# Kernel tuning notes

Hardware: AMD Instinct MI355X
Metric: run time of the kernel (lower is better)

The kernel has to match this reference:

```python
import jax, jax.numpy as jnp
import numpy as np

B, S = 2, 2048
IN, CD = 512, 128
HID, HEADS, DH = 1024, 8, 128
FFN, LAT, L = 4096, 256, 2


def _ln(x, s, b, eps=1e-5):
    m = x.mean(-1, keepdims=True)
    v = x.var(-1, keepdims=True)
    return (x - m) / jnp.sqrt(v + eps) * s + b


def _decay_mask():
    # D[h, n, m] = gamma_h^(n-m) for n >= m else 0; gamma_h = 1 - 2^(-5-h)
    n = jnp.arange(S)
    d = (n[:, None] - n[None, :]).astype(jnp.float32)
    mask = d >= 0
    expo = jnp.where(mask, d, 0.0)
    gammas = 1.0 - 2.0 ** (-5.0 - jnp.arange(HEADS, dtype=jnp.float32))
    return (gammas[:, None, None] ** expo[None]) * mask[None]


def setup_inputs() -> dict:
    key = jax.random.key(0)
    ks = jax.random.split(key, 20)
    f32 = jnp.float32
    def nrm(k, shape, s=0.02):
        return jax.random.normal(k, shape, f32) * s
    return {
        "x": jax.random.normal(ks[0], (B, S, IN), f32),
        "c": jax.random.normal(ks[1], (B, S, CD), f32),
        "W_in": nrm(ks[2], (IN + CD, HID)), "b_in": jnp.zeros((HID,), f32),
        "ln1_s": jnp.ones((L, HID), f32), "ln1_b": jnp.zeros((L, HID), f32),
        "Wq": nrm(ks[3], (L, HID, HID)), "Wk": nrm(ks[4], (L, HID, HID)),
        "Wv": nrm(ks[5], (L, HID, HID)), "Wg": nrm(ks[6], (L, HID, HID)),
        "Wo": nrm(ks[7], (L, HID, HID)),
        "gn_s": jnp.ones((L, HID), f32), "gn_b": jnp.zeros((L, HID), f32),
        "ln2_s": jnp.ones((L, HID), f32), "ln2_b": jnp.zeros((L, HID), f32),
        "W1": nrm(ks[8], (L, HID, FFN)), "b1": jnp.zeros((L, FFN), f32),
        "W2": nrm(ks[9], (L, FFN, HID)), "b2": jnp.zeros((L, HID), f32),
        "lnf_s": jnp.ones((HID,), f32), "lnf_b": jnp.zeros((HID,), f32),
        "W_mu": nrm(ks[10], (HID, LAT)), "b_mu": jnp.zeros((LAT,), f32),
        "W_lv": nrm(ks[11], (HID, LAT)), "b_lv": jnp.zeros((LAT,), f32),
    }


def reference(x, c, W_in, b_in, ln1_s, ln1_b, Wq, Wk, Wv, Wg, Wo, gn_s, gn_b,
              ln2_s, ln2_b, W1, b1, W2, b2, lnf_s, lnf_b, W_mu, b_mu, W_lv, b_lv):
    D = _decay_mask()                        # [H, S, S]
    h = jnp.concatenate([x, c], -1) @ W_in + b_in  # [B, S, HID]
    scale = 1.0 / np.sqrt(DH).astype(np.float32)
    for l in range(L):
        # --- multi-scale retention (parallel form) ---
        xn = _ln(h, ln1_s[l], ln1_b[l])
        q = (xn @ Wq[l]).reshape(B, S, HEADS, DH)
        k = (xn @ Wk[l]).reshape(B, S, HEADS, DH)
        v = (xn @ Wv[l]).reshape(B, S, HEADS, DH)
        scores = jnp.einsum('bnhd,bmhd->bhnm', q, k) * scale
        scores = scores * D[None]            # causal decay weighting
        o = jnp.einsum('bhnm,bmhd->bnhd', scores, v)
        # per-head group norm
        mu_ = o.mean(-1, keepdims=True)
        var_ = o.var(-1, keepdims=True)
        o = (o - mu_) / jnp.sqrt(var_ + 1e-5)
        o = o * gn_s[l].reshape(HEADS, DH) + gn_b[l].reshape(HEADS, DH)
        o = o.reshape(B, S, HID)
        g = jax.nn.silu(xn @ Wg[l])
        h = h + (g * o) @ Wo[l]
        # --- FFN ---
        xn2 = _ln(h, ln2_s[l], ln2_b[l])
        h = h + jax.nn.gelu(xn2 @ W1[l] + b1[l]) @ W2[l] + b2[l]
    h = _ln(h, lnf_s, lnf_b)
    mu = h @ W_mu + b_mu
    raw_logvar = h @ W_lv + b_lv
    std = jax.nn.softplus(0.5 * raw_logvar) + 0.001
    return mu, std
```

## Files before the change

kernel.cpp:

```cpp
#include <hip/hip_runtime.h>
#include <cmath>

typedef __bf16 bf16_t;
typedef __bf16 bf16x8 __attribute__((ext_vector_type(8)));
typedef float f32x4 __attribute__((ext_vector_type(4)));
typedef unsigned int u32x4 __attribute__((ext_vector_type(4)));

namespace {

constexpr int kS = 2048;
constexpr int kTok = 4096;
constexpr int kHid = 1024;
constexpr int kDh = 128;
constexpr float kScale = 0.08838834764831843f;

enum {
  EPI_BF16 = 0,
  EPI_BIAS_F32 = 2,
  EPI_RESID_F32 = 3,
  EPI_BIAS_GELU_BF16 = 4,
  EPI_MULV = 7,
  EPI_PART = 8,
};

__device__ __forceinline__ void gload16(const void* g, void* l) {
  __builtin_amdgcn_global_load_lds(
      (const __attribute__((address_space(1))) void*)g,
      (__attribute__((address_space(3))) void*)l, 16, 0, 0);
}

__global__ __launch_bounds__(256) void build_a0_kernel(
    const float* __restrict__ x, const float* __restrict__ c,
    bf16_t* __restrict__ a0)
{
  int i = blockIdx.x * 256 + threadIdx.x;
  if (i >= kTok * 640) return;
  int t = i / 640;
  int col = i - t * 640;
  float v = (col < 512) ? x[(size_t)t * 512 + col]
                        : c[(size_t)t * 128 + (col - 512)];
  a0[i] = (bf16_t)v;
}

__global__ __launch_bounds__(256) void transpose_cast_kernel(
    const float* __restrict__ src, bf16_t* __restrict__ dst, int K, int N)
{
  __shared__ float tile[32][33];
  int n0 = blockIdx.x * 32, k0 = blockIdx.y * 32;
  int tx = threadIdx.x, ty = threadIdx.y;
#pragma unroll
  for (int ii = 0; ii < 4; ++ii) {
    int r = ty + ii * 8;
    tile[r][tx] = src[(size_t)(k0 + r) * N + (n0 + tx)];
  }
  __syncthreads();
#pragma unroll
  for (int ii = 0; ii < 4; ++ii) {
    int r = ty + ii * 8;
    dst[(size_t)(n0 + r) * K + (k0 + tx)] = (bf16_t)tile[tx][r];
  }
}

__global__ __launch_bounds__(256) void head_transpose_kernel(
    const bf16_t* __restrict__ in, int ld, bf16_t* __restrict__ out)
{
  __shared__ bf16_t tile[32][33];
  int s0 = blockIdx.x * 32;
  int d0 = blockIdx.y * 32;
  int bh = blockIdx.z;
  int b = bh >> 3, h = bh & 7;
  int tx = threadIdx.x & 31, ty = threadIdx.x >> 5;
#pragma unroll
  for (int ii = 0; ii < 4; ++ii) {
    int r = ty + ii * 8;
    tile[r][tx] = in[(size_t)(b * kS + s0 + r) * ld + h * kDh + d0 + tx];
  }
  __syncthreads();
#pragma unroll
  for (int ii = 0; ii < 4; ++ii) {
    int r = ty + ii * 8;
    out[((size_t)bh * kDh + d0 + r) * kS + s0 + tx] = tile[tx][r];
  }
}

__global__ __launch_bounds__(256) void ln_kernel(
    const float* __restrict__ H, const float* __restrict__ s,
    const float* __restrict__ b, bf16_t* __restrict__ out)
{
  const int t = blockIdx.x;
  const int tid = threadIdx.x;
  const float* row = H + (size_t)t * kHid;
  f32x4 x = *(const f32x4*)(row + tid * 4);
  float sum = x[0] + x[1] + x[2] + x[3];
  float ssq = x[0]*x[0] + x[1]*x[1] + x[2]*x[2] + x[3]*x[3];
#pragma unroll
  for (int m = 32; m >= 1; m >>= 1) {
    sum += __shfl_xor(sum, m, 64);
    ssq += __shfl_xor(ssq, m, 64);
  }
  __shared__ float red[8];
  int wave = tid >> 6;
  if ((tid & 63) == 0) { red[wave] = sum; red[4 + wave] = ssq; }
  __syncthreads();
  sum = red[0] + red[1] + red[2] + red[3];
  ssq = red[4] + red[5] + red[6] + red[7];
  float mean = sum * (1.0f / kHid);
  float var = ssq * (1.0f / kHid) - mean * mean;
  float rstd = rsqrtf(var + 1e-5f);
  bf16_t* orow = out + (size_t)t * kHid;
#pragma unroll
  for (int j = 0; j < 4; ++j) {
    int col = tid * 4 + j;
    orow[col] = (bf16_t)((x[j] - mean) * rstd * s[col] + b[col]);
  }
}

__global__ __launch_bounds__(256) void gn_gate_kernel(
    const float* __restrict__ o, const float* __restrict__ gns,
    const float* __restrict__ gnb, bf16_t* __restrict__ g, int ldg)
{
  int idx = blockIdx.x * 4 + (threadIdx.x >> 6);
  int lane = threadIdx.x & 63;
  size_t off = (size_t)idx * kDh;
  float v0 = o[off + lane * 2];
  float v1 = o[off + lane * 2 + 1];
  float sum = v0 + v1, ssq = v0 * v0 + v1 * v1;
#pragma unroll
  for (int m = 32; m >= 1; m >>= 1) {
    sum += __shfl_xor(sum, m, 64);
    ssq += __shfl_xor(ssq, m, 64);
  }
  float mean = sum * (1.0f / kDh);
  float var = ssq * (1.0f / kDh) - mean * mean;
  float rstd = rsqrtf(var + 1e-5f);
  int t = idx >> 3, h = idx & 7;
  int c0 = h * kDh + lane * 2;
  float s0 = gns[c0], s1 = gns[c0 + 1], b0 = gnb[c0], b1 = gnb[c0 + 1];
  size_t goff = (size_t)t * ldg + h * kDh + lane * 2;
  float g0 = (float)g[goff], g1 = (float)g[goff + 1];
  g0 = g0 / (1.0f + __expf(-g0));
  g1 = g1 / (1.0f + __expf(-g1));
  g[goff]     = (bf16_t)(((v0 - mean) * rstd * s0 + b0) * g0);
  g[goff + 1] = (bf16_t)(((v1 - mean) * rstd * s1 + b1) * g1);
}

template <int TM, int EPI>
__global__ __launch_bounds__(256) void gemm_kernel(
    const bf16_t* __restrict__ A, int lda, const bf16_t* __restrict__ Bt, int ldb,
    void* __restrict__ Cv, int ldc, const float* __restrict__ bias,
    const float* __restrict__ bias2, const float* __restrict__ resid,
    int M, int N, int kSpan)
{
  constexpr int MR = TM / 32;
  constexpr int ASEG = TM / 8;
  constexpr int TOT = ASEG + 16;
  constexpr int PER_WAVE = TOT / 4;
  __shared__ bf16_t As[2][TM * 64];
  __shared__ bf16_t Bs[2][128 * 64];
  const int tid = threadIdx.x;
  const int lane = tid & 63;
  const int wave = tid >> 6;
  const int wr = (wave >> 1) * (MR * 16);
  const int wc = (wave & 1) * 64;
  const int bm = blockIdx.x * TM;
  const int bn = blockIdx.y * 128;
  const int kb = blockIdx.z * kSpan;
  const int r_ld = lane >> 3;
  const int cg = ((lane & 7) ^ r_ld) * 8;

  f32x4 acc[MR][4] = {};

  auto stage = [&](int bufi, int t) {
    int k0 = kb + t * 64;
#pragma unroll
    for (int i = 0; i < PER_WAVE; ++i) {
      int seg = wave * PER_WAVE + i;
      if (seg < ASEG) {
        int r = seg * 8 + r_ld;
        gload16(&A[(size_t)(bm + r) * lda + k0 + cg], &As[bufi][seg * 512]);
      } else {
        int s2 = seg - ASEG;
        int r = s2 * 8 + r_ld;
        gload16(&Bt[(size_t)(bn + r) * ldb + k0 + cg], &Bs[bufi][s2 * 512]);
      }
    }
  };
  auto compute = [&](int bufi) {
#pragma unroll
    for (int kk = 0; kk < 64; kk += 32) {
      const int cg0 = (kk >> 3) + (lane >> 4);
      bf16x8 af[MR], bfr[4];
#pragma unroll
      for (int m = 0; m < MR; ++m) {
        int row = wr + m * 16 + (lane & 15);
        af[m] = *(const bf16x8*)&As[bufi][row * 64 + ((cg0 ^ (row & 7)) << 3)];
      }
#pragma unroll
      for (int n = 0; n < 4; ++n) {
        int row = wc + n * 16 + (lane & 15);
        bfr[n] = *(const bf16x8*)&Bs[bufi][row * 64 + ((cg0 ^ (row & 7)) << 3)];
      }
#pragma unroll
      for (int m = 0; m < MR; ++m)
#pragma unroll
        for (int n = 0; n < 4; ++n)
          acc[m][n] = __builtin_amdgcn_mfma_f32_16x16x32_bf16(af[m], bfr[n], acc[m][n], 0, 0, 0);
    }
  };

  const int nt = kSpan >> 6;
  stage(0, 0);
  stage(1, 1);
  for (int t = 0; t < nt; ++t) {
    if (t + 1 < nt) {
      if constexpr (PER_WAVE == 8) asm volatile("s_waitcnt vmcnt(8)" ::: "memory");
      else                         asm volatile("s_waitcnt vmcnt(6)" ::: "memory");
    } else {
      asm volatile("s_waitcnt vmcnt(0)" ::: "memory");
    }
    __builtin_amdgcn_s_barrier();
    compute(t & 1);
    __builtin_amdgcn_s_barrier();
    if (t + 2 < nt) stage(t & 1, t + 2);
  }

  const int cr = (lane >> 4) * 4;
  const int cc = lane & 15;
#pragma unroll
  for (int m = 0; m < MR; ++m) {
#pragma unroll
    for (int n = 0; n < 4; ++n) {
#pragma unroll
      for (int j = 0; j < 4; ++j) {
        int gr = bm + wr + m * 16 + cr + j;
        int gc = bn + wc + n * 16 + cc;
        size_t off = (size_t)gr * ldc + gc;
        float v = acc[m][n][j];
        if constexpr (EPI == EPI_BF16) {
          ((bf16_t*)Cv)[off] = (bf16_t)v;
        } else if constexpr (EPI == EPI_BIAS_F32) {
          ((float*)Cv)[off] = v + bias[gc];
        } else if constexpr (EPI == EPI_RESID_F32) {
          ((float*)Cv)[off] = v + resid[off];
        } else if constexpr (EPI == EPI_BIAS_GELU_BF16) {
          v += bias[gc];
          float u3 = v + 0.044715f * v * v * v;
          float th = tanhf(0.7978845608028654f * u3);
          ((bf16_t*)Cv)[off] = (bf16_t)(0.5f * v * (1.0f + th));
        } else if constexpr (EPI == EPI_PART) {
          ((float*)Cv)[(size_t)blockIdx.z * M * N + off] = v;
        } else if constexpr (EPI == EPI_MULV) {
          if (gc < 256) {
            ((float*)Cv)[(size_t)gr * 256 + gc] = v + bias[gc];
          } else {
            float r2 = 0.5f * (v + bias2[gc - 256]);
            float sp = (r2 > 20.0f) ? r2 : log1pf(__expf(r2));
            ((float*)Cv)[(size_t)4096 * 256 + (size_t)gr * 256 + (gc - 256)] = sp + 0.001f;
          }
        }
      }
    }
  }
}

__global__ __launch_bounds__(256) void ffn2_reduce_kernel(
    const float* __restrict__ P, const float* __restrict__ b2,
    float* __restrict__ H)
{
  int i = blockIdx.x * 256 + threadIdx.x;
  size_t e = (size_t)i * 4;
  int col = (int)(e & 1023);
  f32x4 a = *(const f32x4*)&P[e];
  f32x4 b = *(const f32x4*)&P[(size_t)4096 * 1024 + e];
  f32x4 h = *(const f32x4*)&H[e];
  f32x4 bb = *(const f32x4*)&b2[col];
  f32x4 r = { h[0] + a[0] + b[0] + bb[0], h[1] + a[1] + b[1] + bb[1],
              h[2] + a[2] + b[2] + bb[2], h[3] + a[3] + b[3] + bb[3] };
  *(f32x4*)&H[e] = r;
}

__global__ __launch_bounds__(256) void chunk_state_kernel(
    const bf16_t* __restrict__ KT, const bf16_t* __restrict__ VT,
    bf16_t* __restrict__ U)
{
  __shared__ bf16_t Ka[128][72];
  __shared__ bf16_t Va[128][72];
  const int tid = threadIdx.x, lane = tid & 63, wave = tid >> 6;
  const int t = blockIdx.x, bh = blockIdx.y, h = bh & 7;
  const float lg2g = log2f(1.0f - exp2f(-5.0f - (float)h));
#pragma unroll
  for (int it = 0; it < 4; ++it) {
    int u = tid + it * 256;
    int r = u >> 3, cg = (u & 7) * 8;
    size_t g = ((size_t)bh * kDh + r) * kS + t * 64 + cg;
    *(u32x4*)&Va[r][cg] = *(const u32x4*)&VT[g];
    bf16x8 kv = *(const bf16x8*)&KT[g];
    bf16x8 ks;
#pragma unroll
    for (int j = 0; j < 8; ++j)
      ks[j] = (bf16_t)((float)kv[j] * exp2f((float)(63 - (cg + j)) * lg2g));
    *(bf16x8*)&Ka[r][cg] = ks;
  }
  __syncthreads();
  f32x4 acc[2][8] = {};
#pragma unroll
  for (int kk = 0; kk < 64; kk += 32) {
    bf16x8 af[2], bfr[8];
#pragma unroll
    for (int m = 0; m < 2; ++m)
      af[m] = *(const bf16x8*)&Va[wave * 32 + m * 16 + (lane & 15)][kk + (lane >> 4) * 8];
#pragma unroll
    for (int n = 0; n < 8; ++n)
      bfr[n] = *(const bf16x8*)&Ka[n * 16 + (lane & 15)][kk + (lane >> 4) * 8];
#pragma unroll
    for (int m = 0; m < 2; ++m)
#pragma unroll
      for (int n = 0; n < 8; ++n)
        acc[m][n] = __builtin_amdgcn_mfma_f32_16x16x32_bf16(af[m], bfr[n], acc[m][n], 0, 0, 0);
  }
  size_t base = ((size_t)bh * 32 + t) * 16384;
#pragma unroll
  for (int m = 0; m < 2; ++m)
#pragma unroll
    for (int n = 0; n < 8; ++n)
#pragma unroll
      for (int j = 0; j < 4; ++j) {
        int dv = wave * 32 + m * 16 + (lane >> 4) * 4 + j;
        int dk = n * 16 + (lane & 15);
        U[base + dv * 128 + dk] = (bf16_t)acc[m][n][j];
      }
}

__global__ __launch_bounds__(256) void chunk_scan_kernel(
    const bf16_t* __restrict__ U, bf16_t* __restrict__ S)
{
  int e = blockIdx.x * 256 + threadIdx.x;
  int bh = blockIdx.y, h = bh & 7;
  float d64 = exp2f(64.0f * log2f(1.0f - exp2f(-5.0f - (float)h)));
  float s = 0.0f;
  size_t base = (size_t)bh * 32 * 16384 + e;
  for (int t = 0; t < 32; ++t) {
    size_t idx = base + (size_t)t * 16384;
    float u = (float)U[idx];
    S[idx] = (bf16_t)s;
    s = d64 * s + u;
  }
}

__global__ __launch_bounds__(256) void chunk_out_kernel(
    const bf16_t* __restrict__ QB, const bf16_t* __restrict__ KB, int ldq,
    const bf16_t* __restrict__ VT, const bf16_t* __restrict__ S,
    float* __restrict__ OF)
{
  __shared__ bf16_t Qs[64][136];
  __shared__ bf16_t Ks[64][136];
  __shared__ bf16_t Vs[128][72];
  __shared__ bf16_t Ps[64][72];
  const int tid = threadIdx.x, lane = tid & 63, wave = tid >> 6;
  const int t = blockIdx.x, bh = blockIdx.y;
  const int b = bh >> 3, h = bh & 7;
  const float lg2g = log2f(1.0f - exp2f(-5.0f - (float)h));

#pragma unroll
  for (int it = 0; it < 4; ++it) {
    int u = tid + it * 256;
    int r = u >> 4, cg = (u & 15) * 8;
    size_t g = ((size_t)b * kS + t * 64 + r) * ldq + h * kDh + cg;
    *(u32x4*)&Qs[r][cg] = *(const u32x4*)&QB[g];
    *(u32x4*)&Ks[r][cg] = *(const u32x4*)&KB[g];
    int rv = u >> 3, cv = (u & 7) * 8;
    *(u32x4*)&Vs[rv][cv] = *(const u32x4*)&VT[((size_t)bh * kDh + rv) * kS + t * 64 + cv];
  }
  __syncthreads();

  f32x4 sf[4] = {};
#pragma unroll
  for (int kk = 0; kk < 128; kk += 32) {
    bf16x8 aq = *(const bf16x8*)&Qs[wave * 16 + (lane & 15)][kk + (lane >> 4) * 8];
#pragma unroll
    for (int c2 = 0; c2 < 4; ++c2) {
      bf16x8 bk = *(const bf16x8*)&Ks[c2 * 16 + (lane & 15)][kk + (lane >> 4) * 8];
      sf[c2] = __builtin_amdgcn_mfma_f32_16x16x32_bf16(aq, bk, sf[c2], 0, 0, 0);
    }
  }
#pragma unroll
  for (int c2 = 0; c2 < 4; ++c2)
#pragma unroll
    for (int j = 0; j < 4; ++j) {
      int nl = wave * 16 + (lane >> 4) * 4 + j;
      int ml = c2 * 16 + (lane & 15);
      int d = nl - ml;
      float w = (d >= 0) ? kScale * exp2f((float)d * lg2g) : 0.0f;
      Ps[nl][ml] = (bf16_t)(sf[c2][j] * w);
    }
  __syncthreads();

  f32x4 oa[8] = {}, oi[8] = {};
#pragma unroll
  for (int ks = 0; ks < 64; ks += 32) {
    bf16x8 ap = *(const bf16x8*)&Ps[wave * 16 + (lane & 15)][ks + (lane >> 4) * 8];
#pragma unroll
    for (int dt = 0; dt < 8; ++dt) {
      bf16x8 bv = *(const bf16x8*)&Vs[dt * 16 + (lane & 15)][ks + (lane >> 4) * 8];
      oa[dt] = __builtin_amdgcn_mfma_f32_16x16x32_bf16(ap, bv, oa[dt], 0, 0, 0);
    }
  }
  size_t sbase = ((size_t)bh * 32 + t) * 16384;
#pragma unroll
  for (int kk = 0; kk < 128; kk += 32) {
    bf16x8 aq = *(const bf16x8*)&Qs[wave * 16 + (lane & 15)][kk + (lane >> 4) * 8];
#pragma unroll
    for (int dt = 0; dt < 8; ++dt) {
      bf16x8 bs = *(const bf16x8*)&S[sbase + (size_t)(dt * 16 + (lane & 15)) * 128 + kk + (lane >> 4) * 8];
      oi[dt] = __builtin_amdgcn_mfma_f32_16x16x32_bf16(aq, bs, oi[dt], 0, 0, 0);
    }
  }
#pragma unroll
  for (int dt = 0; dt < 8; ++dt)
#pragma unroll
    for (int j = 0; j < 4; ++j) {
      int nl = wave * 16 + (lane >> 4) * 4 + j;
      float gf = kScale * exp2f((float)(nl + 1) * lg2g);
      OF[((size_t)b * kS + t * 64 + nl) * kHid + h * kDh + dt * 16 + (lane & 15)] =
          oa[dt][j] + gf * oi[dt][j];
    }
}

template <int TM>
void launch_gemm(int epi, const bf16_t* A, int lda, const bf16_t* Bt, int ldb,
                 void* C, int ldc, const float* bias, const float* bias2,
                 const float* resid, int M, int N, int K, int ksplit, hipStream_t st)
{
  dim3 g(M / TM, N / 128, ksplit), b(256);
  int kSpan = K / ksplit;
  switch (epi) {
    case EPI_BF16:           gemm_kernel<TM, EPI_BF16><<<g, b, 0, st>>>(A, lda, Bt, ldb, C, ldc, bias, bias2, resid, M, N, kSpan); break;
    case EPI_BIAS_F32:       gemm_kernel<TM, EPI_BIAS_F32><<<g, b, 0, st>>>(A, lda, Bt, ldb, C, ldc, bias, bias2, resid, M, N, kSpan); break;
    case EPI_RESID_F32:      gemm_kernel<TM, EPI_RESID_F32><<<g, b, 0, st>>>(A, lda, Bt, ldb, C, ldc, bias, bias2, resid, M, N, kSpan); break;
    case EPI_BIAS_GELU_BF16: gemm_kernel<TM, EPI_BIAS_GELU_BF16><<<g, b, 0, st>>>(A, lda, Bt, ldb, C, ldc, bias, bias2, resid, M, N, kSpan); break;
    case EPI_PART:           gemm_kernel<TM, EPI_PART><<<g, b, 0, st>>>(A, lda, Bt, ldb, C, ldc, bias, bias2, resid, M, N, kSpan); break;
    case EPI_MULV:           gemm_kernel<TM, EPI_MULV><<<g, b, 0, st>>>(A, lda, Bt, ldb, C, ldc, bias, bias2, resid, M, N, kSpan); break;
  }
}

void launch_transpose(const float* src, bf16_t* dst, int K, int N, hipStream_t st) {
  transpose_cast_kernel<<<dim3(N / 32, K / 32), dim3(32, 8), 0, st>>>(src, dst, K, N);
}

}

extern "C" void kernel_launch(void* const* d_in, const int* in_sizes, int n_in,
                              void* d_out, int out_size, void* d_ws, size_t ws_size,
                              hipStream_t stream) {
  const float* x     = (const float*)d_in[0];
  const float* c     = (const float*)d_in[1];
  const float* W_in  = (const float*)d_in[2];
  const float* b_in  = (const float*)d_in[3];
  const float* ln1_s = (const float*)d_in[4];
  const float* ln1_b = (const float*)d_in[5];
  const float* Wq    = (const float*)d_in[6];
  const float* Wk    = (const float*)d_in[7];
  const float* Wv    = (const float*)d_in[8];
  const float* Wg    = (const float*)d_in[9];
  const float* Wo    = (const float*)d_in[10];
  const float* gn_s  = (const float*)d_in[11];
  const float* gn_b  = (const float*)d_in[12];
  const float* ln2_s = (const float*)d_in[13];
  const float* ln2_b = (const float*)d_in[14];
  const float* W1    = (const float*)d_in[15];
  const float* b1    = (const float*)d_in[16];
  const float* W2    = (const float*)d_in[17];
  const float* b2    = (const float*)d_in[18];
  const float* lnf_s = (const float*)d_in[19];
  const float* lnf_b = (const float*)d_in[20];
  const float* W_mu  = (const float*)d_in[21];
  const float* b_mu  = (const float*)d_in[22];
  const float* W_lv  = (const float*)d_in[23];
  const float* b_lv  = (const float*)d_in[24];

  char* p = (char*)d_ws;
  bf16_t* WT   = (bf16_t*)p; p += (size_t)4096 * 1024 * 2;
  bf16_t* A0   = (bf16_t*)p; p += (size_t)4096 * 640 * 2;
  float*  H    = (float*) p; p += (size_t)4096 * 1024 * 4;
  bf16_t* XN   = (bf16_t*)p; p += (size_t)4096 * 1024 * 2;
  bf16_t* QKVG = (bf16_t*)p; p += (size_t)4096 * 4096 * 2;
  bf16_t* Sb   = (bf16_t*)p; p += (size_t)16 * 32 * 16384 * 2;
  float*  OF   = (float*) p; p += (size_t)4096 * 1024 * 4;
  bf16_t* F1 = QKVG;
  bf16_t* KT = WT;
  bf16_t* VT = XN;
  bf16_t* Ub = (bf16_t*)OF;
  float*  PART = (float*)Sb;

  build_a0_kernel<<<dim3((kTok * 640 + 255) / 256), dim3(256), 0, stream>>>(x, c, A0);
  launch_transpose(W_in, WT, 640, 1024, stream);
  launch_gemm<64>(EPI_BIAS_F32, A0, 640, WT, 640, H, 1024, b_in, nullptr, nullptr,
                  4096, 1024, 640, 1, stream);

  for (int l = 0; l < 2; ++l) {
    const size_t wsq = (size_t)l * 1024 * 1024;
    ln_kernel<<<dim3(4096), dim3(256), 0, stream>>>(H, ln1_s + l * 1024, ln1_b + l * 1024, XN);

    launch_transpose(Wq + wsq, WT,                      1024, 1024, stream);
    launch_transpose(Wk + wsq, WT + ((size_t)1 << 20),  1024, 1024, stream);
    launch_transpose(Wv + wsq, WT + ((size_t)2 << 20),  1024, 1024, stream);
    launch_transpose(Wg + wsq, WT + ((size_t)3 << 20),  1024, 1024, stream);
    launch_gemm<128>(EPI_BF16, XN, 1024, WT, 1024, QKVG, 4096, nullptr, nullptr, nullptr,
                     4096, 4096, 1024, 1, stream);

    head_transpose_kernel<<<dim3(64, 4, 16), dim3(256), 0, stream>>>(QKVG + 1024, 4096, KT);
    head_transpose_kernel<<<dim3(64, 4, 16), dim3(256), 0, stream>>>(QKVG + 2048, 4096, VT);
    chunk_state_kernel<<<dim3(32, 16), dim3(256), 0, stream>>>(KT, VT, Ub);
    chunk_scan_kernel<<<dim3(64, 16), dim3(256), 0, stream>>>(Ub, (bf16_t*)Sb);
    chunk_out_kernel<<<dim3(32, 16), dim3(256), 0, stream>>>(QKVG, QKVG + 1024, 4096, VT, (bf16_t*)Sb, OF);

    gn_gate_kernel<<<dim3(8192), dim3(256), 0, stream>>>(OF, gn_s + l * 1024, gn_b + l * 1024,
                                                         QKVG + 3072, 4096);

    launch_transpose(Wo + wsq, WT, 1024, 1024, stream);
    launch_gemm<64>(EPI_RESID_F32, QKVG + 3072, 4096, WT, 1024, H, 1024, nullptr, nullptr, H,
                    4096, 1024, 1024, 1, stream);

    ln_kernel<<<dim3(4096), dim3(256), 0, stream>>>(H, ln2_s + l * 1024, ln2_b + l * 1024, XN);
    launch_transpose(W1 + (size_t)l * 1024 * 4096, WT, 1024, 4096, stream);
    launch_gemm<128>(EPI_BIAS_GELU_BF16, XN, 1024, WT, 1024, F1, 4096, b1 + l * 4096, nullptr, nullptr,
                     4096, 4096, 1024, 1, stream);
    launch_transpose(W2 + (size_t)l * 4096 * 1024, WT, 4096, 1024, stream);
    launch_gemm<128>(EPI_PART, F1, 4096, WT, 4096, PART, 1024, nullptr, nullptr, nullptr,
                     4096, 1024, 4096, 2, stream);
    ffn2_reduce_kernel<<<dim3(4096), dim3(256), 0, stream>>>(PART, b2 + l * 1024, H);
  }

  ln_kernel<<<dim3(4096), dim3(256), 0, stream>>>(H, lnf_s, lnf_b, XN);
  launch_transpose(W_mu, WT, 1024, 256, stream);
  launch_transpose(W_lv, WT + (size_t)256 * 1024, 1024, 256, stream);
  launch_gemm<64>(EPI_MULV, XN, 1024, WT, 1024, d_out, 512, b_mu, b_lv, nullptr,
                  4096, 512, 1024, 1, stream);
}
```

Before: 552.9 us.

## Add 256x256-tile 8-wave GEMM with interleaved staging for large projections

Adds a new GEMM kernel using 256x256 output tiles with 512 threads (8 waves), double-buffered LDS staging through global_load_lds, and prefetch loads interleaved between four MFMA phases using setprio and sched barriers. It replaces the 128-tile GEMM for the QKVG projection, the FFN1 GELU GEMM and the split-K FFN2 GEMM. The larger tiles raise arithmetic intensity and reuse of LDS data, and the interleaving aims to hide global load latency behind MFMA work. The cost is 128 KB of LDS per block and fewer blocks: 256 for the N=4096 GEMMs and 128 for FFN2, which may not fill all CUs on the device.

```diff
diff --git a/kernel.cpp b/kernel.cpp
--- a/kernel.cpp
+++ b/kernel.cpp
@@ -27,6 +27,10 @@
   __builtin_amdgcn_global_load_lds(
       (const __attribute__((address_space(1))) void*)g,
       (__attribute__((address_space(3))) void*)l, 16, 0, 0);
+}
+
+__device__ __forceinline__ f32x4 mfma16(bf16x8 a, bf16x8 b, f32x4 c) {
+  return __builtin_amdgcn_mfma_f32_16x16x32_bf16(a, b, c, 0, 0, 0);
 }
 
 __global__ __launch_bounds__(256) void build_a0_kernel(
@@ -204,7 +208,7 @@
       for (int m = 0; m < MR; ++m)
 #pragma unroll
         for (int n = 0; n < 4; ++n)
-          acc[m][n] = __builtin_amdgcn_mfma_f32_16x16x32_bf16(af[m], bfr[n], acc[m][n], 0, 0, 0);
+          acc[m][n] = mfma16(af[m], bfr[n], acc[m][n]);
     }
   };
 
@@ -263,6 +267,181 @@
   }
 }
 
+template <int EPI>
+__global__ __launch_bounds__(512, 2) void gemm256_kernel(
+    const bf16_t* __restrict__ A, int lda, const bf16_t* __restrict__ Bt, int ldb,
+    void* __restrict__ Cv, int ldc, const float* __restrict__ bias,
+    int M, int N, int kSpan)
+{
+  __shared__ bf16_t As[2][256 * 64];
+  __shared__ bf16_t Bs[2][256 * 64];
+  const int tid = threadIdx.x;
+  const int lane = tid & 63;
+  const int wave = tid >> 6;
+  const int wm = wave >> 2;
+  const int wn = wave & 3;
+  const int bm = blockIdx.x * 256;
+  const int bn = blockIdx.y * 256;
+  const int kb = blockIdx.z * kSpan;
+  const int r_ld = lane >> 3;
+  const int cgs = ((lane & 7) ^ r_ld) * 8;
+  const int rl15 = lane & 15, rl7 = lane & 7, rhi = lane >> 4;
+
+  f32x4 acc[8][4] = {};
+
+  auto stageA = [&](int bufi, int t, int h) {
+    int k0 = kb + t * 64;
+#pragma unroll
+    for (int i = 0; i < 2; ++i) {
+      int seg = h * 16 + wave * 2 + i;
+      int r = seg * 8 + r_ld;
+      gload16(&A[(size_t)(bm + r) * lda + k0 + cgs], &As[bufi][seg * 512]);
+    }
+  };
+  auto stageB = [&](int bufi, int t, int h) {
+    int k0 = kb + t * 64;
+#pragma unroll
+    for (int i = 0; i < 2; ++i) {
+      int seg = h * 16 + wave * 2 + i;
+      int r = seg * 8 + r_ld;
+      gload16(&Bt[(size_t)(bn + r) * ldb + k0 + cgs], &Bs[bufi][seg * 512]);
+    }
+  };
+  auto lda_frag = [&](int bufi, int mf, int kk) -> bf16x8 {
+    int row = wm * 128 + mf * 16 + rl15;
+    int cg0 = (kk >> 3) + rhi;
+    return *(const bf16x8*)&As[bufi][row * 64 + ((cg0 ^ rl7) << 3)];
+  };
+  auto ldb_frag = [&](int bufi, int nf, int kk) -> bf16x8 {
+    int row = wn * 64 + nf * 16 + rl15;
+    int cg0 = (kk >> 3) + rhi;
+    return *(const bf16x8*)&Bs[bufi][row * 64 + ((cg0 ^ rl7) << 3)];
+  };
+
+  const int nt = kSpan >> 6;
+  stageA(0, 0, 0); stageB(0, 0, 0); stageB(0, 0, 1); stageA(0, 0, 1);
+
+  bf16x8 bk0[4], bk1[4], af[4];
+
+  for (int t = 0; t < nt - 1; ++t) {
+    const int cb = t & 1, nb = cb ^ 1;
+    asm volatile("s_waitcnt vmcnt(2)" ::: "memory");
+    __builtin_amdgcn_s_barrier();
+#pragma unroll
+    for (int nf = 0; nf < 4; ++nf) bk0[nf] = ldb_frag(cb, nf, 0);
+#pragma unroll
+    for (int mf = 0; mf < 4; ++mf) af[mf] = lda_frag(cb, mf, 0);
+    stageA(nb, t + 1, 0); stageB(nb, t + 1, 0);
+    asm volatile("s_waitcnt lgkmcnt(0)" ::: "memory");
+    __builtin_amdgcn_sched_barrier(0);
+    __builtin_amdgcn_s_setprio(1);
+#pragma unroll
+    for (int mf = 0; mf < 4; ++mf)
+#pragma unroll
+      for (int nf = 0; nf < 4; ++nf)
+        acc[mf][nf] = mfma16(af[mf], bk0[nf], acc[mf][nf]);
+    __builtin_amdgcn_s_setprio(0);
+    __builtin_amdgcn_s_barrier();
+#pragma unroll
+    for (int nf = 0; nf < 4; ++nf) bk1[nf] = ldb_frag(cb, nf, 32);
+#pragma unroll
+    for (int mf = 0; mf < 4; ++mf) af[mf] = lda_frag(cb, mf, 32);
+    stageB(nb, t + 1, 1);
+    asm volatile("s_waitcnt lgkmcnt(0)" ::: "memory");
+    __builtin_amdgcn_sched_barrier(0);
+    __builtin_amdgcn_s_setprio(1);
+#pragma unroll
+    for (int mf = 0; mf < 4; ++mf)
+#pragma unroll
+      for (int nf = 0; nf < 4; ++nf)
+        acc[mf][nf] = mfma16(af[mf], bk1[nf], acc[mf][nf]);
+    __builtin_amdgcn_s_setprio(0);
+    asm volatile("s_waitcnt vmcnt(6)" ::: "memory");
+    __builtin_amdgcn_s_barrier();
+#pragma unroll
+    for (int mf = 0; mf < 4; ++mf) af[mf] = lda_frag(cb, 4 + mf, 0);
+    stageA(nb, t + 1, 1);
+    asm volatile("s_waitcnt lgkmcnt(0)" ::: "memory");
+    __builtin_amdgcn_sched_barrier(0);
+    __builtin_amdgcn_s_setprio(1);
+#pragma unroll
+    for (int mf = 0; mf < 4; ++mf)
+#pragma unroll
+      for (int nf = 0; nf < 4; ++nf)
+        acc[4 + mf][nf] = mfma16(af[mf], bk0[nf], acc[4 + mf][nf]);
+    __builtin_amdgcn_s_setprio(0);
+    __builtin_amdgcn_s_barrier();
+#pragma unroll
+    for (int mf = 0; mf < 4; ++mf) af[mf] = lda_frag(cb, 4 + mf, 32);
+    asm volatile("s_waitcnt lgkmcnt(0)" ::: "memory");
+    __builtin_amdgcn_sched_barrier(0);
+    __builtin_amdgcn_s_setprio(1);
+#pragma unroll
+    for (int mf = 0; mf < 4; ++mf)
+#pragma unroll
+      for (int nf = 0; nf < 4; ++nf)
+        acc[4 + mf][nf] = mfma16(af[mf], bk1[nf], acc[4 + mf][nf]);
+    __builtin_amdgcn_s_setprio(0);
+  }
+
+  {
+    const int cb = (nt - 1) & 1;
+    asm volatile("s_waitcnt vmcnt(0)" ::: "memory");
+    __builtin_amdgcn_s_barrier();
+#pragma unroll
+    for (int nf = 0; nf < 4; ++nf) bk0[nf] = ldb_frag(cb, nf, 0);
+#pragma unroll
+    for (int nf = 0; nf < 4; ++nf) bk1[nf] = ldb_frag(cb, nf, 32);
+#pragma unroll
+    for (int half = 0; half < 2; ++half) {
+#pragma unroll
+      for (int mf = 0; mf < 4; ++mf) af[mf] = lda_frag(cb, half * 4 + mf, 0);
+      asm volatile("s_waitcnt lgkmcnt(0)" ::: "memory");
+      __builtin_amdgcn_sched_barrier(0);
+#pragma unroll
+      for (int mf = 0; mf < 4; ++mf)
+#pragma unroll
+        for (int nf = 0; nf < 4; ++nf)
+          acc[half * 4 + mf][nf] = mfma16(af[mf], bk0[nf], acc[half * 4 + mf][nf]);
+#pragma unroll
+      for (int mf = 0; mf < 4; ++mf) af[mf] = lda_frag(cb, half * 4 + mf, 32);
+      asm volatile("s_waitcnt lgkmcnt(0)" ::: "memory");
+      __builtin_amdgcn_sched_barrier(0);
+#pragma unroll
+      for (int mf = 0; mf < 4; ++mf)
+#pragma unroll
+        for (int nf = 0; nf < 4; ++nf)
+          acc[half * 4 + mf][nf] = mfma16(af[mf], bk1[nf], acc[half * 4 + mf][nf]);
+    }
+  }
+
+  const int cr = rhi * 4;
+  const int cc = rl15;
+#pragma unroll
+  for (int mf = 0; mf < 8; ++mf) {
+#pragma unroll
+    for (int nf = 0; nf < 4; ++nf) {
+#pragma unroll
+      for (int j = 0; j < 4; ++j) {
+        int gr = bm + wm * 128 + mf * 16 + cr + j;
+        int gc = bn + wn * 64 + nf * 16 + cc;
+        size_t off = (size_t)gr * ldc + gc;
+        float v = acc[mf][nf][j];
+        if constexpr (EPI == EPI_BF16) {
+          ((bf16_t*)Cv)[off] = (bf16_t)v;
+        } else if constexpr (EPI == EPI_BIAS_GELU_BF16) {
+          v += bias[gc];
+          float u3 = v + 0.044715f * v * v * v;
+          float th = tanhf(0.7978845608028654f * u3);
+          ((bf16_t*)Cv)[off] = (bf16_t)(0.5f * v * (1.0f + th));
+        } else if constexpr (EPI == EPI_PART) {
+          ((float*)Cv)[(size_t)blockIdx.z * M * N + off] = v;
+        }
+      }
+    }
+  }
+}
+
 __global__ __launch_bounds__(256) void ffn2_reduce_kernel(
     const float* __restrict__ P, const float* __restrict__ b2,
     float* __restrict__ H)
@@ -316,7 +495,7 @@
     for (int m = 0; m < 2; ++m)
 #pragma unroll
       for (int n = 0; n < 8; ++n)
-        acc[m][n] = __builtin_amdgcn_mfma_f32_16x16x32_bf16(af[m], bfr[n], acc[m][n], 0, 0, 0);
+        acc[m][n] = mfma16(af[m], bfr[n], acc[m][n]);
   }
   size_t base = ((size_t)bh * 32 + t) * 16384;
 #pragma unroll
@@ -380,7 +559,7 @@
 #pragma unroll
     for (int c2 = 0; c2 < 4; ++c2) {
       bf16x8 bk = *(const bf16x8*)&Ks[c2 * 16 + (lane & 15)][kk + (lane >> 4) * 8];
-      sf[c2] = __builtin_amdgcn_mfma_f32_16x16x32_bf16(aq, bk, sf[c2], 0, 0, 0);
+      sf[c2] = mfma16(aq, bk, sf[c2]);
     }
   }
 #pragma unroll
@@ -402,7 +581,7 @@
 #pragma unroll
     for (int dt = 0; dt < 8; ++dt) {
       bf16x8 bv = *(const bf16x8*)&Vs[dt * 16 + (lane & 15)][ks + (lane >> 4) * 8];
-      oa[dt] = __builtin_amdgcn_mfma_f32_16x16x32_bf16(ap, bv, oa[dt], 0, 0, 0);
+      oa[dt] = mfma16(ap, bv, oa[dt]);
     }
   }
   size_t sbase = ((size_t)bh * 32 + t) * 16384;
@@ -412,7 +591,7 @@
 #pragma unroll
     for (int dt = 0; dt < 8; ++dt) {
       bf16x8 bs = *(const bf16x8*)&S[sbase + (size_t)(dt * 16 + (lane & 15)) * 128 + kk + (lane >> 4) * 8];
-      oi[dt] = __builtin_amdgcn_mfma_f32_16x16x32_bf16(aq, bs, oi[dt], 0, 0, 0);
+      oi[dt] = mfma16(aq, bs, oi[dt]);
     }
   }
 #pragma unroll
@@ -505,8 +684,8 @@
     launch_transpose(Wk + wsq, WT + ((size_t)1 << 20),  1024, 1024, stream);
     launch_transpose(Wv + wsq, WT + ((size_t)2 << 20),  1024, 1024, stream);
     launch_transpose(Wg + wsq, WT + ((size_t)3 << 20),  1024, 1024, stream);
-    launch_gemm<128>(EPI_BF16, XN, 1024, WT, 1024, QKVG, 4096, nullptr, nullptr, nullptr,
-                     4096, 4096, 1024, 1, stream);
+    gemm256_kernel<EPI_BF16><<<dim3(16, 16, 1), dim3(512), 0, stream>>>(
+        XN, 1024, WT, 1024, QKVG, 4096, nullptr, 4096, 4096, 1024);
 
     head_transpose_kernel<<<dim3(64, 4, 16), dim3(256), 0, stream>>>(QKVG + 1024, 4096, KT);
     head_transpose_kernel<<<dim3(64, 4, 16), dim3(256), 0, stream>>>(QKVG + 2048, 4096, VT);
@@ -523,11 +702,11 @@
 
     ln_kernel<<<dim3(4096), dim3(256), 0, stream>>>(H, ln2_s + l * 1024, ln2_b + l * 1024, XN);
     launch_transpose(W1 + (size_t)l * 1024 * 4096, WT, 1024, 4096, stream);
-    launch_gemm<128>(EPI_BIAS_GELU_BF16, XN, 1024, WT, 1024, F1, 4096, b1 + l * 4096, nullptr, nullptr,
-                     4096, 4096, 1024, 1, stream);
+    gemm256_kernel<EPI_BIAS_GELU_BF16><<<dim3(16, 16, 1), dim3(512), 0, stream>>>(
+        XN, 1024, WT, 1024, F1, 4096, b1 + l * 4096, 4096, 4096, 1024);
     launch_transpose(W2 + (size_t)l * 4096 * 1024, WT, 4096, 1024, stream);
-    launch_gemm<128>(EPI_PART, F1, 4096, WT, 4096, PART, 1024, nullptr, nullptr, nullptr,
-                     4096, 1024, 4096, 2, stream);
+    gemm256_kernel<EPI_PART><<<dim3(16, 4, 2), dim3(512), 0, stream>>>(
+        F1, 4096, WT, 4096, PART, 1024, nullptr, 4096, 1024, 2048);
     ffn2_reduce_kernel<<<dim3(4096), dim3(256), 0, stream>>>(PART, b2 + l * 1024, H);
   }
 
```

New measurement: 566.9 us. 1.03x slower.
